# Kernel optimization log

Measured on AMD Instinct MI355X. Metric: run time of the kernel, lower is better.

## Reference

```python
import jax, jax.numpy as jnp
import numpy as np

D_MODEL = 1024
N_HEADS = 16
HEAD_DIM = D_MODEL // N_HEADS
BATCH = 2
SEQ = 2048


def setup_inputs() -> dict:
    key = jax.random.key(0)
    ks = jax.random.split(key, 9)
    s = 1.0 / np.sqrt(D_MODEL)
    inp = {
        "x": jax.random.normal(ks[0], (BATCH, SEQ, D_MODEL), dtype=jnp.float32),
        "Wq": jax.random.uniform(ks[1], (D_MODEL, D_MODEL), jnp.float32, -s, s),
        "bq": jax.random.uniform(ks[2], (D_MODEL,), jnp.float32, -s, s),
        "Wk": jax.random.uniform(ks[3], (D_MODEL, D_MODEL), jnp.float32, -s, s),
        "bk": jax.random.uniform(ks[4], (D_MODEL,), jnp.float32, -s, s),
        "Wv": jax.random.uniform(ks[5], (D_MODEL, D_MODEL), jnp.float32, -s, s),
        "bv": jax.random.uniform(ks[6], (D_MODEL,), jnp.float32, -s, s),
        "Wo": jax.random.uniform(ks[7], (D_MODEL, D_MODEL), jnp.float32, -s, s),
        "bo": jax.random.uniform(ks[8], (D_MODEL,), jnp.float32, -s, s),
    }
    return inp


def reference(x, Wq, bq, Wk, bk, Wv, bv, Wo, bo):
    B, S, _ = x.shape
    # projections -> [B, H, S, Dh]
    def proj(W, b):
        y = jnp.einsum('bsd,df->bsf', x, W) + b
        return y.reshape(B, S, N_HEADS, HEAD_DIM).transpose(0, 2, 1, 3)
    q = proj(Wq, bq)
    k = proj(Wk, bk)
    v = proj(Wv, bv)
    scores = jnp.einsum('bhqd,bhkd->bhqk', q, k) / jnp.sqrt(jnp.float32(HEAD_DIM))
    mask = jnp.tril(jnp.ones((S, S), dtype=bool))  # [S, S] causal mask
    scores = jnp.where(mask, scores, -jnp.inf)
    weights = jax.nn.softmax(scores, axis=-1)
    h = jnp.einsum('bhqk,bhkd->bhqd', weights, v)
    h = h.transpose(0, 2, 1, 3).reshape(B, S, N_HEADS * HEAD_DIM)
    return jnp.einsum('bsd,df->bsf', h, Wo) + bo
```

## Files before the change

### kernel.cpp

```cpp
#include <hip/hip_runtime.h>
#include <hip/hip_bf16.h>
#include <cmath>

#define D_MODEL 1024
#define NHEADS 16
#define HDIM 64
#define BATCH 2
#define SEQ 2048
#define MROWS (BATCH*SEQ)
#define KDIM 1024

typedef unsigned short ushort_t;
typedef unsigned int uint32;
typedef __attribute__((ext_vector_type(8))) short short8;
typedef __attribute__((ext_vector_type(4))) float floatx4;

#define QSCALE 0.1803368801111204f
#define EXP2F(x) __builtin_amdgcn_exp2f(x)

__device__ __forceinline__ ushort_t f2bf(float x) {
    union { float f; uint32 u; } v; v.f = x;
    uint32 r = v.u + 0x7FFFu + ((v.u >> 16) & 1u);
    return (ushort_t)(r >> 16);
}

__device__ __forceinline__ uint32 pkbf(float a, float b) {
    union { __hip_bfloat162 h2; uint32 u; } v;
    v.h2 = __float22bfloat162_rn(make_float2(a, b));
    return v.u;
}

__device__ __forceinline__ void glds16(const void* g, void* l) {
    __builtin_amdgcn_global_load_lds(
        (const __attribute__((address_space(1))) void*)g,
        (__attribute__((address_space(3))) void*)l, 16, 0, 0);
}

__global__ __launch_bounds__(256)
void cvt_all(const float* __restrict__ x, const float* __restrict__ W0,
             const float* __restrict__ W1, const float* __restrict__ W2,
             const float* __restrict__ W3, ushort_t* __restrict__ xb,
             ushort_t* __restrict__ WtQKV, ushort_t* __restrict__ WtO)
{
    const int z = blockIdx.z;
    if (z == 4) {
        size_t idx = ((size_t)blockIdx.y * 32 + blockIdx.x) * 256 + threadIdx.x;
        #pragma unroll
        for (int l = 0; l < 4; ++l) {
            size_t i = ((size_t)l * 262144 + idx) * 4;
            float4 v = *(const float4*)(x + i);
            uint2 o;
            o.x = pkbf(v.x, v.y);
            o.y = pkbf(v.z, v.w);
            *(uint2*)(xb + i) = o;
        }
        return;
    }
    __shared__ float tl[32][33];
    const float* W = (z == 0) ? W0 : (z == 1) ? W1 : (z == 2) ? W2 : W3;
    ushort_t* out = (z < 3) ? (WtQKV + (size_t)z * D_MODEL * KDIM) : WtO;
    const int k0 = blockIdx.x * 32, n0 = blockIdx.y * 32;
    const int tx = threadIdx.x & 31, ty = threadIdx.x >> 5;
    #pragma unroll
    for (int i = 0; i < 4; ++i)
        tl[ty + i * 8][tx] = W[(size_t)(k0 + ty + i * 8) * D_MODEL + n0 + tx];
    __syncthreads();
    #pragma unroll
    for (int i = 0; i < 4; ++i)
        out[(size_t)(n0 + ty + i * 8) * KDIM + k0 + tx] = f2bf(tl[tx][ty + i * 8]);
}

template<int BN>
__global__ __launch_bounds__(256)
void gemm_mfma(const ushort_t* __restrict__ A, const ushort_t* __restrict__ Bt,
               const float* __restrict__ b0, const float* __restrict__ b1,
               const float* __restrict__ b2, float* __restrict__ Cf,
               ushort_t* __restrict__ Qb, ushort_t* __restrict__ Kb,
               ushort_t* __restrict__ Vb, int mode)
{
    constexpr int NT = BN / 32;
    constexpr int BC = BN / 32;
    __shared__ ushort_t As[128 * 64];
    __shared__ ushort_t Bs[BN * 64];

    const int tid = threadIdx.x;
    const int w = tid >> 6, lane = tid & 63;
    const int quad = lane >> 4, col = lane & 15;
    const int m0 = blockIdx.y * 128, n0 = blockIdx.x * BN;
    const int mbase = (w & 1) * 64, nbase = (w >> 1) * (BN / 2);

    floatx4 zero = {0.f, 0.f, 0.f, 0.f};
    floatx4 acc[4][NT];
    #pragma unroll
    for (int i = 0; i < 4; ++i)
        #pragma unroll
        for (int j = 0; j < NT; ++j) acc[i][j] = zero;

    #pragma unroll 1
    for (int k0 = 0; k0 < KDIM; k0 += 64) {
        #pragma unroll
        for (int i = 0; i < 4; ++i) {
            int c = (w * 4 + i) * 64 + lane;
            int row = c >> 3;
            int kc = (c & 7) ^ (row & 7);
            glds16(A + (size_t)(m0 + row) * KDIM + k0 + kc * 8, As + (w * 4 + i) * 512);
        }
        #pragma unroll
        for (int i = 0; i < BC; ++i) {
            int c = (w * BC + i) * 64 + lane;
            int row = c >> 3;
            int kc = (c & 7) ^ (row & 7);
            glds16(Bt + (size_t)(n0 + row) * KDIM + k0 + kc * 8, Bs + (w * BC + i) * 512);
        }
        __syncthreads();
        #pragma unroll
        for (int ks = 0; ks < 2; ++ks) {
            short8 af[4], bfr[NT];
            const int kc = ks * 4 + quad;
            #pragma unroll
            for (int mt = 0; mt < 4; ++mt) {
                int r = mbase + mt * 16 + col;
                af[mt] = *(const short8*)(As + ((size_t)r * 8 + (kc ^ (r & 7))) * 8);
            }
            #pragma unroll
            for (int nt = 0; nt < NT; ++nt) {
                int r = nbase + nt * 16 + col;
                bfr[nt] = *(const short8*)(Bs + ((size_t)r * 8 + (kc ^ (r & 7))) * 8);
            }
            #pragma unroll
            for (int mt = 0; mt < 4; ++mt)
                #pragma unroll
                for (int nt = 0; nt < NT; ++nt)
                    acc[mt][nt] = __builtin_amdgcn_mfma_f32_16x16x32_bf16(
                        af[mt], bfr[nt], acc[mt][nt], 0, 0, 0);
        }
        __syncthreads();
    }

    if (mode == 0) {
        #pragma unroll
        for (int mt = 0; mt < 4; ++mt)
            #pragma unroll
            for (int nt = 0; nt < NT; ++nt) {
                int n = n0 + nbase + nt * 16 + col;
                float bb = b0[n];
                #pragma unroll
                for (int r = 0; r < 4; ++r) {
                    int m = m0 + mbase + mt * 16 + quad * 4 + r;
                    Cf[(size_t)m * D_MODEL + n] = acc[mt][nt][r] + bb;
                }
            }
    } else {
        const int which = n0 >> 10;
        const float* bp = (which == 0) ? b0 : (which == 1) ? b1 : b2;
        if (which < 2) {
            ushort_t* outp = (which == 0) ? Qb : Kb;
            const float scl = (which == 0) ? QSCALE : 1.0f;
            #pragma unroll
            for (int mt = 0; mt < 4; ++mt)
                #pragma unroll
                for (int nt = 0; nt < NT; ++nt) {
                    int nn = (n0 + nbase + nt * 16 + col) & 1023;
                    float bb = bp[nn];
                    int h = nn >> 6, d = nn & 63;
                    #pragma unroll
                    for (int r = 0; r < 4; ++r) {
                        int m = m0 + mbase + mt * 16 + quad * 4 + r;
                        int b = m >> 11, s = m & 2047;
                        outp[((size_t)(b * NHEADS + h) * SEQ + s) * HDIM + d] =
                            f2bf((acc[mt][nt][r] + bb) * scl);
                    }
                }
        } else {
            #pragma unroll
            for (int mt = 0; mt < 4; ++mt)
                #pragma unroll
                for (int nt = 0; nt < NT; ++nt) {
                    int nn = (n0 + nbase + nt * 16 + col) & 1023;
                    float bb = bp[nn];
                    int h = nn >> 6, d = nn & 63;
                    int mb = m0 + mbase + mt * 16 + quad * 4;
                    int b = mb >> 11, s = mb & 2047;
                    uint2 pw;
                    pw.x = pkbf(acc[mt][nt][0] + bb, acc[mt][nt][1] + bb);
                    pw.y = pkbf(acc[mt][nt][2] + bb, acc[mt][nt][3] + bb);
                    *(uint2*)(Vb + ((size_t)(b * NHEADS + h) * HDIM + d) * SEQ + s) = pw;
                }
        }
    }
}

__global__ __launch_bounds__(256)
void attn_mfma(const ushort_t* __restrict__ Q, const ushort_t* __restrict__ K,
               const ushort_t* __restrict__ Vt, ushort_t* __restrict__ H)
{
    __shared__ ushort_t Qs[64 * 64];
    __shared__ ushort_t Ks[64 * 64];
    __shared__ ushort_t Vs[64 * 64];
    ushort_t* Ps = Qs;

    const int tid = threadIdx.x;
    const int w = tid >> 6, lane = tid & 63;
    const int quad = lane >> 4, col = lane & 15;
    const int blk = blockIdx.x;
    const int bh = (blk & 7) * 4 + ((blk >> 3) & 3);
    const int pair = blk >> 5;
    const size_t base = (size_t)bh * SEQ * HDIM;
    const ushort_t* Kb = K + base;
    const ushort_t* Vb = Vt + base;
    const int b = bh >> 4, h = bh & 15;

    const int c0 = (w * 2 + 0) * 64 + lane;
    const int c1 = (w * 2 + 1) * 64 + lane;
    const int r0 = c0 >> 3, o0 = ((c0 & 7) ^ (r0 & 7)) * 8;
    const int r1 = c1 >> 3, o1 = ((c1 & 7) ^ (r1 & 7)) * 8;

    const int qloc = w * 16 + col;
    const int rq = qloc;
    const floatx4 zero = {0.f, 0.f, 0.f, 0.f};

    #pragma unroll 1
    for (int pi = 0; pi < 2; ++pi) {
        const int qt = pi ? pair : 31 - pair;
        const int q0 = qt * 64;

        __syncthreads();
        #pragma unroll
        for (int i = 0; i < 2; ++i) {
            int c = (w * 2 + i) * 64 + lane;
            int row = c >> 3, kc = (c & 7) ^ (row & 7);
            glds16(Q + base + (size_t)(q0 + row) * HDIM + kc * 8, Qs + (w * 2 + i) * 512);
        }
        __syncthreads();
        short8 bq[2];
        #pragma unroll
        for (int ks = 0; ks < 2; ++ks) {
            int kc = ks * 4 + quad;
            bq[ks] = *(const short8*)(Qs + ((size_t)rq * 8 + (kc ^ (rq & 7))) * 8);
        }

        uint4 kr0 = *(const uint4*)(Kb + (size_t)r0 * HDIM + o0);
        uint4 kr1 = *(const uint4*)(Kb + (size_t)r1 * HDIM + o1);
        uint4 vr0 = *(const uint4*)(Vb + (size_t)r0 * SEQ + o0);
        uint4 vr1 = *(const uint4*)(Vb + (size_t)r1 * SEQ + o1);

        floatx4 o[4];
        #pragma unroll
        for (int j = 0; j < 4; ++j) o[j] = zero;
        float lreg = 0.f;

        const int nt = qt + 1;
        #pragma unroll 1
        for (int t = 0; t < nt; ++t) {
            __syncthreads();
            *(uint4*)(Ks + (size_t)c0 * 8) = kr0;
            *(uint4*)(Ks + (size_t)c1 * 8) = kr1;
            *(uint4*)(Vs + (size_t)c0 * 8) = vr0;
            *(uint4*)(Vs + (size_t)c1 * 8) = vr1;
            __syncthreads();
            if (t < nt - 1) {
                const int k0n = (t + 1) * 64;
                kr0 = *(const uint4*)(Kb + (size_t)(k0n + r0) * HDIM + o0);
                kr1 = *(const uint4*)(Kb + (size_t)(k0n + r1) * HDIM + o1);
                vr0 = *(const uint4*)(Vb + (size_t)r0 * SEQ + k0n + o0);
                vr1 = *(const uint4*)(Vb + (size_t)r1 * SEQ + k0n + o1);
            }

            floatx4 sc[4];
            #pragma unroll
            for (int j = 0; j < 4; ++j) sc[j] = zero;
            #pragma unroll
            for (int ks = 0; ks < 2; ++ks) {
                const int kc = ks * 4 + quad;
                #pragma unroll
                for (int j = 0; j < 4; ++j) {
                    int rk = j * 16 + col;
                    short8 ak = *(const short8*)(Ks + ((size_t)rk * 8 + (kc ^ (rk & 7))) * 8);
                    sc[j] = __builtin_amdgcn_mfma_f32_16x16x32_bf16(ak, bq[ks], sc[j], 0, 0, 0);
                }
            }

            if (t == nt - 1) {
                #pragma unroll
                for (int j = 0; j < 4; ++j)
                    #pragma unroll
                    for (int r = 0; r < 4; ++r)
                        if (j * 16 + quad * 4 + r > qloc) sc[j][r] = -INFINITY;
            }

            float ls = 0.f;
            #pragma unroll
            for (int j = 0; j < 4; ++j) {
                float p0 = EXP2F(sc[j][0]);
                float p1 = EXP2F(sc[j][1]);
                float p2 = EXP2F(sc[j][2]);
                float p3 = EXP2F(sc[j][3]);
                ls += (p0 + p1) + (p2 + p3);
                uint2 pw;
                pw.x = pkbf(p0, p1);
                pw.y = pkbf(p2, p3);
                int c = 2 * j + (quad >> 1);
                *(uint2*)(Ps + ((size_t)rq * 8 + (c ^ (rq & 7))) * 8 + (quad & 1) * 4) = pw;
            }
            lreg += ls;

            #pragma unroll
            for (int ks = 0; ks < 2; ++ks) {
                const int kc = ks * 4 + quad;
                short8 bp = *(const short8*)(Ps + ((size_t)rq * 8 + (kc ^ (rq & 7))) * 8);
                #pragma unroll
                for (int j = 0; j < 4; ++j) {
                    int rv = j * 16 + col;
                    short8 av = *(const short8*)(Vs + ((size_t)rv * 8 + (kc ^ (rv & 7))) * 8);
                    o[j] = __builtin_amdgcn_mfma_f32_16x16x32_bf16(av, bp, o[j], 0, 0, 0);
                }
            }
        }

        lreg += __shfl_xor(lreg, 16);
        lreg += __shfl_xor(lreg, 32);

        const float linv = 1.f / lreg;
        const size_t rowb = ((size_t)(b * SEQ + q0 + qloc)) * D_MODEL + h * HDIM;
        #pragma unroll
        for (int j = 0; j < 4; ++j) {
            uint2 pw;
            pw.x = pkbf(o[j][0] * linv, o[j][1] * linv);
            pw.y = pkbf(o[j][2] * linv, o[j][3] * linv);
            *(uint2*)(H + rowb + j * 16 + quad * 4) = pw;
        }
    }
}

extern "C" void kernel_launch(void* const* d_in, const int* in_sizes, int n_in,
                              void* d_out, int out_size, void* d_ws, size_t ws_size,
                              hipStream_t stream)
{
    (void)in_sizes; (void)n_in; (void)out_size; (void)ws_size;
    const float* x  = (const float*)d_in[0];
    const float* Wq = (const float*)d_in[1];
    const float* bq = (const float*)d_in[2];
    const float* Wk = (const float*)d_in[3];
    const float* bk = (const float*)d_in[4];
    const float* Wv = (const float*)d_in[5];
    const float* bv = (const float*)d_in[6];
    const float* Wo = (const float*)d_in[7];
    const float* bo = (const float*)d_in[8];

    const size_t E = (size_t)MROWS * D_MODEL;
    ushort_t* xb    = (ushort_t*)d_ws;
    ushort_t* WtQKV = xb + E;
    ushort_t* WtO   = WtQKV + 3 * (size_t)D_MODEL * KDIM;
    ushort_t* Qb    = WtO + (size_t)D_MODEL * KDIM;
    ushort_t* Kb    = Qb + E;
    ushort_t* Vb    = Kb + E;
    ushort_t* Hb    = Vb + E;

    cvt_all<<<dim3(32, 32, 5), 256, 0, stream>>>(x, Wq, Wk, Wv, Wo, xb, WtQKV, WtO);
    gemm_mfma<128><<<dim3(24, 32), 256, 0, stream>>>(xb, WtQKV, bq, bk, bv,
                                                     nullptr, Qb, Kb, Vb, 1);
    attn_mfma<<<dim3(512), 256, 0, stream>>>(Qb, Kb, Vb, Hb);
    gemm_mfma<64><<<dim3(16, 32), 256, 0, stream>>>(Hb, WtO, bo, nullptr, nullptr,
                                                    (float*)d_out, nullptr, nullptr, nullptr, 0);
}
```

Baseline: 191.6 us.

## Add dedicated QKV GEMM kernel with 2 waves computing 64x128 each

Replaces the generic 256-thread GEMM for the fused QKV projection with a 128-thread kernel in which each of two wavefronts computes a 64x128 tile (4x8 MFMA tiles) instead of four waves each doing 64x64. This raises per-wave register reuse of A/B fragments and halves LDS reads per MFMA, at the cost of a larger accumulator footprint (128 floats per lane) and lower occupancy per block. The output GEMM is simplified to drop the unused mode branch.

```diff
diff --git a/kernel.cpp b/kernel.cpp
--- a/kernel.cpp
+++ b/kernel.cpp
@@ -70,13 +70,104 @@
         out[(size_t)(n0 + ty + i * 8) * KDIM + k0 + tx] = f2bf(tl[tx][ty + i * 8]);
 }
 
+__global__ __launch_bounds__(128, 2)
+void gemm_qkv(const ushort_t* __restrict__ A, const ushort_t* __restrict__ Bt,
+              const float* __restrict__ b0, const float* __restrict__ b1,
+              const float* __restrict__ b2, ushort_t* __restrict__ Qb,
+              ushort_t* __restrict__ Kb, ushort_t* __restrict__ Vb)
+{
+    __shared__ ushort_t As[128 * 64];
+    __shared__ ushort_t Bs[128 * 64];
+
+    const int tid = threadIdx.x;
+    const int w = tid >> 6, lane = tid & 63;
+    const int quad = lane >> 4, col = lane & 15;
+    const int m0 = blockIdx.y * 128, n0 = blockIdx.x * 128;
+
+    floatx4 zero = {0.f, 0.f, 0.f, 0.f};
+    floatx4 acc[4][8];
+    #pragma unroll
+    for (int i = 0; i < 4; ++i)
+        #pragma unroll
+        for (int j = 0; j < 8; ++j) acc[i][j] = zero;
+
+    #pragma unroll 1
+    for (int k0 = 0; k0 < KDIM; k0 += 64) {
+        #pragma unroll
+        for (int i = 0; i < 8; ++i) {
+            int c = i * 128 + tid;
+            int row = c >> 3;
+            int kc = (c & 7) ^ (row & 7);
+            glds16(A  + (size_t)(m0 + row) * KDIM + k0 + kc * 8, As + (i * 128 + w * 64) * 8);
+            glds16(Bt + (size_t)(n0 + row) * KDIM + k0 + kc * 8, Bs + (i * 128 + w * 64) * 8);
+        }
+        __syncthreads();
+        #pragma unroll
+        for (int ks = 0; ks < 2; ++ks) {
+            short8 af[4], bfr[8];
+            const int kc = ks * 4 + quad;
+            #pragma unroll
+            for (int mt = 0; mt < 4; ++mt) {
+                int r = w * 64 + mt * 16 + col;
+                af[mt] = *(const short8*)(As + ((size_t)r * 8 + (kc ^ (r & 7))) * 8);
+            }
+            #pragma unroll
+            for (int nt = 0; nt < 8; ++nt) {
+                int r = nt * 16 + col;
+                bfr[nt] = *(const short8*)(Bs + ((size_t)r * 8 + (kc ^ (r & 7))) * 8);
+            }
+            #pragma unroll
+            for (int mt = 0; mt < 4; ++mt)
+                #pragma unroll
+                for (int nt = 0; nt < 8; ++nt)
+                    acc[mt][nt] = __builtin_amdgcn_mfma_f32_16x16x32_bf16(
+                        af[mt], bfr[nt], acc[mt][nt], 0, 0, 0);
+        }
+        __syncthreads();
+    }
+
+    const int which = n0 >> 10;
+    const float* bp = (which == 0) ? b0 : (which == 1) ? b1 : b2;
+    if (which < 2) {
+        ushort_t* outp = (which == 0) ? Qb : Kb;
+        const float scl = (which == 0) ? QSCALE : 1.0f;
+        #pragma unroll
+        for (int mt = 0; mt < 4; ++mt)
+            #pragma unroll
+            for (int nt = 0; nt < 8; ++nt) {
+                int nn = (n0 + nt * 16 + col) & 1023;
+                float bb = bp[nn];
+                int h = nn >> 6, d = nn & 63;
+                #pragma unroll
+                for (int r = 0; r < 4; ++r) {
+                    int m = m0 + w * 64 + mt * 16 + quad * 4 + r;
+                    int b = m >> 11, s = m & 2047;
+                    outp[((size_t)(b * NHEADS + h) * SEQ + s) * HDIM + d] =
+                        f2bf((acc[mt][nt][r] + bb) * scl);
+                }
+            }
+    } else {
+        #pragma unroll
+        for (int mt = 0; mt < 4; ++mt)
+            #pragma unroll
+            for (int nt = 0; nt < 8; ++nt) {
+                int nn = (n0 + nt * 16 + col) & 1023;
+                float bb = bp[nn];
+                int h = nn >> 6, d = nn & 63;
+                int mb = m0 + w * 64 + mt * 16 + quad * 4;
+                int b = mb >> 11, s = mb & 2047;
+                uint2 pw;
+                pw.x = pkbf(acc[mt][nt][0] + bb, acc[mt][nt][1] + bb);
+                pw.y = pkbf(acc[mt][nt][2] + bb, acc[mt][nt][3] + bb);
+                *(uint2*)(Vb + ((size_t)(b * NHEADS + h) * HDIM + d) * SEQ + s) = pw;
+            }
+    }
+}
+
 template<int BN>
 __global__ __launch_bounds__(256)
 void gemm_mfma(const ushort_t* __restrict__ A, const ushort_t* __restrict__ Bt,
-               const float* __restrict__ b0, const float* __restrict__ b1,
-               const float* __restrict__ b2, float* __restrict__ Cf,
-               ushort_t* __restrict__ Qb, ushort_t* __restrict__ Kb,
-               ushort_t* __restrict__ Vb, int mode)
+               const float* __restrict__ b0, float* __restrict__ Cf)
 {
     constexpr int NT = BN / 32;
     constexpr int BC = BN / 32;
@@ -137,57 +228,18 @@
         __syncthreads();
     }
 
-    if (mode == 0) {
-        #pragma unroll
-        for (int mt = 0; mt < 4; ++mt)
-            #pragma unroll
-            for (int nt = 0; nt < NT; ++nt) {
-                int n = n0 + nbase + nt * 16 + col;
-                float bb = b0[n];
-                #pragma unroll
-                for (int r = 0; r < 4; ++r) {
-                    int m = m0 + mbase + mt * 16 + quad * 4 + r;
-                    Cf[(size_t)m * D_MODEL + n] = acc[mt][nt][r] + bb;
-                }
-            }
-    } else {
-        const int which = n0 >> 10;
-        const float* bp = (which == 0) ? b0 : (which == 1) ? b1 : b2;
-        if (which < 2) {
-            ushort_t* outp = (which == 0) ? Qb : Kb;
-            const float scl = (which == 0) ? QSCALE : 1.0f;
-            #pragma unroll
-            for (int mt = 0; mt < 4; ++mt)
-                #pragma unroll
-                for (int nt = 0; nt < NT; ++nt) {
-                    int nn = (n0 + nbase + nt * 16 + col) & 1023;
-                    float bb = bp[nn];
-                    int h = nn >> 6, d = nn & 63;
-                    #pragma unroll
-                    for (int r = 0; r < 4; ++r) {
-                        int m = m0 + mbase + mt * 16 + quad * 4 + r;
-                        int b = m >> 11, s = m & 2047;
-                        outp[((size_t)(b * NHEADS + h) * SEQ + s) * HDIM + d] =
-                            f2bf((acc[mt][nt][r] + bb) * scl);
-                    }
-                }
-        } else {
-            #pragma unroll
-            for (int mt = 0; mt < 4; ++mt)
-                #pragma unroll
-                for (int nt = 0; nt < NT; ++nt) {
-                    int nn = (n0 + nbase + nt * 16 + col) & 1023;
-                    float bb = bp[nn];
-                    int h = nn >> 6, d = nn & 63;
-                    int mb = m0 + mbase + mt * 16 + quad * 4;
-                    int b = mb >> 11, s = mb & 2047;
-                    uint2 pw;
-                    pw.x = pkbf(acc[mt][nt][0] + bb, acc[mt][nt][1] + bb);
-                    pw.y = pkbf(acc[mt][nt][2] + bb, acc[mt][nt][3] + bb);
-                    *(uint2*)(Vb + ((size_t)(b * NHEADS + h) * HDIM + d) * SEQ + s) = pw;
-                }
-        }
-    }
+    #pragma unroll
+    for (int mt = 0; mt < 4; ++mt)
+        #pragma unroll
+        for (int nt = 0; nt < NT; ++nt) {
+            int n = n0 + nbase + nt * 16 + col;
+            float bb = b0[n];
+            #pragma unroll
+            for (int r = 0; r < 4; ++r) {
+                int m = m0 + mbase + mt * 16 + quad * 4 + r;
+                Cf[(size_t)m * D_MODEL + n] = acc[mt][nt][r] + bb;
+            }
+        }
 }
 
 __global__ __launch_bounds__(256)
@@ -357,9 +409,7 @@
     ushort_t* Hb    = Vb + E;
 
     cvt_all<<<dim3(32, 32, 5), 256, 0, stream>>>(x, Wq, Wk, Wv, Wo, xb, WtQKV, WtO);
-    gemm_mfma<128><<<dim3(24, 32), 256, 0, stream>>>(xb, WtQKV, bq, bk, bv,
-                                                     nullptr, Qb, Kb, Vb, 1);
+    gemm_qkv<<<dim3(24, 32), 128, 0, stream>>>(xb, WtQKV, bq, bk, bv, Qb, Kb, Vb);
     attn_mfma<<<dim3(512), 256, 0, stream>>>(Qb, Kb, Vb, Hb);
-    gemm_mfma<64><<<dim3(16, 32), 256, 0, stream>>>(Hb, WtO, bo, nullptr, nullptr,
-                                                    (float*)d_out, nullptr, nullptr, nullptr, 0);
-}
+    gemm_mfma<64><<<dim3(16, 32), 256, 0, stream>>>(Hb, WtO, bo, (float*)d_out);
+}
```

New measurement: 181.5 us. -5.2%, faster.
